# Performance work log

Measured on AMD Instinct MI355X. Metric: run time of the kernel, lower is better.

The kernel has to match this reference:

```python
import jax, jax.numpy as jnp
import numpy as np

N, K, D, H = 8192, 32, 128, 256

def setup_inputs() -> dict:
    key = jax.random.key(0)
    ks = jax.random.split(key, 12)
    x = jax.random.normal(ks[0], (N, D), dtype=jnp.float32)
    chosen = jax.random.randint(ks[1], (N, K), 0, N, dtype=jnp.int32)
    # column 0 = the node's own index (matches neighbors[0] == current in the torch code)
    nbrs = jnp.concatenate([jnp.arange(N, dtype=jnp.int32)[:, None], chosen], axis=1)
    t = jax.random.normal(ks[2], (N,), dtype=jnp.float32)
    e_hat = jax.random.normal(ks[3], (N,), dtype=jnp.float32)
    def lin(k, fan_in, fan_out):
        k1, k2 = jax.random.split(k)
        s = 1.0 / np.sqrt(fan_in)
        W = jax.random.uniform(k1, (fan_in, fan_out), minval=-s, maxval=s, dtype=jnp.float32)
        bb = jax.random.uniform(k2, (fan_out,), minval=-s, maxval=s, dtype=jnp.float32)
        return W, bb
    W1, b1 = lin(ks[4], 2 * D, H)
    W2, b2 = lin(ks[5], H, H)
    W3, b3 = lin(ks[6], H, 1)
    b = jnp.float32(1.0)
    return {"x": x, "nbrs": nbrs, "t": t, "e_hat": e_hat,
            "W1": W1, "b1": b1, "W2": W2, "b2": b2, "W3": W3, "b3": b3, "b": b}

def reference(x, nbrs, t, e_hat, W1, b1, W2, b2, W3, b3, b):
    n, d = x.shape
    cur = nbrs[:, 0]          # [n] node's own index
    chosen = nbrs[:, 1:]      # [n, K] neighbor indices
    k = chosen.shape[1]
    z_i = x[cur]              # [n, d]
    z_j = x[chosen]           # [n, K, d] ragged gather (regular degree)
    z_concat = jnp.concatenate(
        [jnp.broadcast_to(z_i[:, None, :], (n, k, d)), z_j], axis=-1)  # [n, K, 2d]
    h = jax.nn.relu(z_concat @ W1 + b1)
    h = jax.nn.relu(h @ W2 + b2)
    mlp_neigh = (h @ W3 + b3)[..., 0]                     # [n, K]
    scores = jax.nn.softmax(b * jnp.abs(mlp_neigh), axis=1)  # per-node softmax
    prop_res = t[chosen] - e_hat[chosen]                  # [n, K]
    w = mlp_neigh * scores                                # [n, K]
    Y_pred = jnp.sum(prop_res * w, axis=1)                # [n]
    pairwise = jnp.zeros((n, n), dtype=x.dtype).at[cur[:, None], chosen].set(w)
    pairwise = pairwise.at[cur, cur].set(0.0)             # zero self-weight last, as in torch
    return Y_pred, pairwise
```

## Files before the change

kernel.cpp:

```cpp
#include <hip/hip_runtime.h>

typedef short s8v __attribute__((ext_vector_type(8)));
typedef float f4v __attribute__((ext_vector_type(4)));

#define NN 8192
#define KN 32
#define DD 128
#define HH 256

static __device__ __forceinline__ unsigned short f2bf(float f) {
    union { float f; unsigned u; } v; v.f = f;
    unsigned r = v.u + 0x7fffu + ((v.u >> 16) & 1u);
    return (unsigned short)(r >> 16);
}
static __device__ __forceinline__ float bf2f(unsigned short h) {
    union { unsigned u; float f; } v; v.u = ((unsigned)h) << 16;
    return v.f;
}

__global__ __launch_bounds__(256) void prep_kernel(
    const float* __restrict__ W1, const float* __restrict__ W2,
    unsigned short* __restrict__ W1sh, unsigned short* __restrict__ W1sl,
    unsigned short* __restrict__ W2s)
{
    int tid = blockIdx.x * 256 + threadIdx.x;
    if (tid < 128 * 512) {
        int k = tid >> 9;
        int n = tid & 511;
        float w = (n < 256) ? W1[k * 256 + n] : W1[(128 + k) * 256 + (n - 256)];
        unsigned short hi = f2bf(w);
        float lo = w - bf2f(hi);
        int idx = ((k >> 5) * 512 + n) * 32 + (k & 31);
        W1sh[idx] = hi;
        W1sl[idx] = f2bf(lo);
    } else {
        int t2 = tid - 128 * 512;
        int k = t2 >> 8;
        int n = t2 & 255;
        W2s[((k >> 5) * 256 + n) * 32 + (k & 31)] = f2bf(W2[k * 256 + n]);
    }
}

__global__ __launch_bounds__(256) void pq_kernel(
    const float* __restrict__ x, const unsigned short* __restrict__ W1sh,
    const unsigned short* __restrict__ W1sl, const float* __restrict__ b1,
    float* __restrict__ P, unsigned short* __restrict__ Q)
{
    __shared__ unsigned short Ah[64 * 136];
    __shared__ unsigned short Al[64 * 136];
    int t  = threadIdx.x;
    int r0 = blockIdx.x * 64;
    int n0 = blockIdx.y * 256;

    {
        int m   = (t & 15) | ((t >> 6) << 4);
        int seg = (t >> 4) & 3;
        const float* xr = x + (r0 + m) * DD + seg * 32;
        #pragma unroll
        for (int it = 0; it < 4; ++it) {
            f4v v0 = *(const f4v*)(xr + it * 8);
            f4v v1 = *(const f4v*)(xr + it * 8 + 4);
            s8v hh, ll;
            #pragma unroll
            for (int e = 0; e < 8; ++e) {
                float v = (e < 4) ? v0[e] : v1[e - 4];
                unsigned short hi = f2bf(v);
                hh[e] = (short)hi;
                ll[e] = (short)f2bf(v - bf2f(hi));
            }
            int c = seg * 32 + it * 8;
            *(s8v*)(Ah + m * 136 + c) = hh;
            *(s8v*)(Al + m * 136 + c) = ll;
        }
    }
    __syncthreads();

    int lane = t & 63, wn = t >> 6, l15 = lane & 15, q = lane >> 4;
    f4v acc[4][4];
    #pragma unroll
    for (int mt = 0; mt < 4; ++mt)
        #pragma unroll
        for (int nt = 0; nt < 4; ++nt) acc[mt][nt] = (f4v){0.f, 0.f, 0.f, 0.f};

    #pragma unroll
    for (int kt = 0; kt < 4; ++kt) {
        s8v ah[4], al[4], bh[4], bl[4];
        #pragma unroll
        for (int mt = 0; mt < 4; ++mt) {
            int m = mt * 16 + l15;
            ah[mt] = *(const s8v*)(Ah + m * 136 + kt * 32 + q * 8);
            al[mt] = *(const s8v*)(Al + m * 136 + kt * 32 + q * 8);
        }
        #pragma unroll
        for (int nt = 0; nt < 4; ++nt) {
            int n = n0 + wn * 64 + nt * 16 + l15;
            int idx = (kt * 512 + n) * 32 + q * 8;
            bh[nt] = *(const s8v*)(W1sh + idx);
            bl[nt] = *(const s8v*)(W1sl + idx);
        }
        #pragma unroll
        for (int mt = 0; mt < 4; ++mt)
            #pragma unroll
            for (int nt = 0; nt < 4; ++nt) {
                acc[mt][nt] = __builtin_amdgcn_mfma_f32_16x16x32_bf16(ah[mt], bh[nt], acc[mt][nt], 0, 0, 0);
                acc[mt][nt] = __builtin_amdgcn_mfma_f32_16x16x32_bf16(ah[mt], bl[nt], acc[mt][nt], 0, 0, 0);
                acc[mt][nt] = __builtin_amdgcn_mfma_f32_16x16x32_bf16(al[mt], bh[nt], acc[mt][nt], 0, 0, 0);
            }
    }

    #pragma unroll
    for (int nt = 0; nt < 4; ++nt) {
        int cg = n0 + wn * 64 + nt * 16 + l15;
        if (cg < 256) {
            float bias = b1[cg];
            #pragma unroll
            for (int mt = 0; mt < 4; ++mt)
                #pragma unroll
                for (int r = 0; r < 4; ++r) {
                    int row = r0 + mt * 16 + q * 4 + r;
                    P[row * 256 + cg] = acc[mt][nt][r] + bias;
                }
        } else {
            int cq = cg - 256;
            #pragma unroll
            for (int mt = 0; mt < 4; ++mt)
                #pragma unroll
                for (int r = 0; r < 4; ++r) {
                    int row = r0 + mt * 16 + q * 4 + r;
                    Q[row * 256 + cq] = f2bf(acc[mt][nt][r]);
                }
        }
    }
}

__global__ __launch_bounds__(256) void main_kernel(
    const float* __restrict__ P, const unsigned short* __restrict__ Q,
    const unsigned short* __restrict__ W2s,
    const float* __restrict__ b2, const float* __restrict__ W3,
    const int* __restrict__ nbrs, const float* __restrict__ t_arr,
    const float* __restrict__ e_hat, const float* __restrict__ b3p,
    const float* __restrict__ bscal, float* __restrict__ out)
{
    __shared__ unsigned short A[64 * 264];
    __shared__ float mlpbuf[64][4];
    __shared__ float wbuf_w[2][32];
    __shared__ int   wbuf_j[2][32];
    int t = threadIdx.x;
    int node0 = blockIdx.x * 2;
    float* PW = out + NN;

    {
        int m   = (t & 15) | ((t >> 6) << 4);
        int seg = (t >> 4) & 3;
        int g = node0 + (m >> 5);
        int i = nbrs[g * 33];
        int j = nbrs[g * 33 + 1 + (m & 31)];
        const float* Pr = P + i * 256 + seg * 64;
        const unsigned short* Qr = Q + j * 256 + seg * 64;
        #pragma unroll
        for (int it = 0; it < 8; ++it) {
            f4v p0 = *(const f4v*)(Pr + it * 8);
            f4v p1 = *(const f4v*)(Pr + it * 8 + 4);
            s8v qv = *(const s8v*)(Qr + it * 8);
            s8v hv;
            #pragma unroll
            for (int e = 0; e < 8; ++e) {
                float pv = (e < 4) ? p0[e] : p1[e - 4];
                float v = pv + bf2f((unsigned short)qv[e]);
                v = v > 0.f ? v : 0.f;
                hv[e] = (short)f2bf(v);
            }
            *(s8v*)(A + m * 264 + seg * 64 + it * 8) = hv;
        }
    }
    __syncthreads();

    int lane = t & 63, wn = t >> 6, l15 = lane & 15, q = lane >> 4;
    f4v acc[4][4];
    #pragma unroll
    for (int mt = 0; mt < 4; ++mt)
        #pragma unroll
        for (int nt = 0; nt < 4; ++nt) acc[mt][nt] = (f4v){0.f, 0.f, 0.f, 0.f};

    #pragma unroll
    for (int kt = 0; kt < 8; ++kt) {
        s8v a[4], b[4];
        #pragma unroll
        for (int mt = 0; mt < 4; ++mt)
            a[mt] = *(const s8v*)(A + (mt * 16 + l15) * 264 + kt * 32 + q * 8);
        #pragma unroll
        for (int nt = 0; nt < 4; ++nt) {
            int n = wn * 64 + nt * 16 + l15;
            b[nt] = *(const s8v*)(W2s + (kt * 256 + n) * 32 + q * 8);
        }
        #pragma unroll
        for (int mt = 0; mt < 4; ++mt)
            #pragma unroll
            for (int nt = 0; nt < 4; ++nt)
                acc[mt][nt] = __builtin_amdgcn_mfma_f32_16x16x32_bf16(a[mt], b[nt], acc[mt][nt], 0, 0, 0);
    }

    float p[4][4];
    #pragma unroll
    for (int mt = 0; mt < 4; ++mt)
        #pragma unroll
        for (int r = 0; r < 4; ++r) p[mt][r] = 0.f;
    #pragma unroll
    for (int nt = 0; nt < 4; ++nt) {
        int c = wn * 64 + nt * 16 + l15;
        float bb = b2[c], w3 = W3[c];
        #pragma unroll
        for (int mt = 0; mt < 4; ++mt)
            #pragma unroll
            for (int r = 0; r < 4; ++r) {
                float v = acc[mt][nt][r] + bb;
                v = v > 0.f ? v : 0.f;
                p[mt][r] += v * w3;
            }
    }
    #pragma unroll
    for (int off = 1; off < 16; off <<= 1)
        #pragma unroll
        for (int mt = 0; mt < 4; ++mt)
            #pragma unroll
            for (int r = 0; r < 4; ++r)
                p[mt][r] += __shfl_xor(p[mt][r], off, 64);
    if (l15 == 0) {
        #pragma unroll
        for (int mt = 0; mt < 4; ++mt)
            #pragma unroll
            for (int r = 0; r < 4; ++r)
                mlpbuf[mt * 16 + q * 4 + r][wn] = p[mt][r];
    }
    __syncthreads();

    if (t < 128) {
        int node = t >> 6;
        int k = t & 63;
        if (k < 32) {
            int g = node0 + node;
            int m = node * 32 + k;
            float mlp = mlpbuf[m][0] + mlpbuf[m][1] + mlpbuf[m][2] + mlpbuf[m][3] + b3p[0];
            float aabs = bscal[0] * fabsf(mlp);
            float amax = aabs;
            #pragma unroll
            for (int off = 1; off < 32; off <<= 1)
                amax = fmaxf(amax, __shfl_xor(amax, off, 64));
            float e = __expf(aabs - amax);
            float s = e;
            #pragma unroll
            for (int off = 1; off < 32; off <<= 1)
                s += __shfl_xor(s, off, 64);
            float w = mlp * (e / s);

            int j = nbrs[g * 33 + 1 + k];
            float prop = t_arr[j] - e_hat[j];
            float yp = prop * w;
            #pragma unroll
            for (int off = 1; off < 32; off <<= 1)
                yp += __shfl_xor(yp, off, 64);
            if (k == 0) out[g] = yp;

            int curg = nbrs[g * 33];
            bool write = (j != curg);
            for (int kk = 0; kk < 32; ++kk) {
                int jv = __shfl(j, kk, 64);
                if (kk > k && jv == j) write = false;
            }
            wbuf_w[node][k] = w;
            wbuf_j[node][k] = write ? j : -1;
        }
    }
    __syncthreads();

    float* img = (float*)A;
    #pragma unroll 1
    for (int row = 0; row < 2; ++row) {
        f4v z = (f4v){0.f, 0.f, 0.f, 0.f};
        #pragma unroll
        for (int i = 0; i < 8; ++i)
            *(f4v*)(img + t * 4 + i * 1024) = z;
        __syncthreads();
        if (t < 32) {
            int j = wbuf_j[row][t];
            if (j >= 0) img[j] = wbuf_w[row][t];
        }
        __syncthreads();
        int cur = nbrs[(node0 + row) * 33];
        float* dst = PW + (long)cur * NN;
        #pragma unroll
        for (int i = 0; i < 8; ++i) {
            f4v v = *(const f4v*)(img + t * 4 + i * 1024);
            __builtin_nontemporal_store(v, (f4v*)(dst + t * 4 + i * 1024));
        }
    }
}

extern "C" void kernel_launch(void* const* d_in, const int* in_sizes, int n_in,
                              void* d_out, int out_size, void* d_ws, size_t ws_size,
                              hipStream_t stream) {
    const float* x     = (const float*)d_in[0];
    const int*   nbrs  = (const int*)d_in[1];
    const float* t     = (const float*)d_in[2];
    const float* e_hat = (const float*)d_in[3];
    const float* W1    = (const float*)d_in[4];
    const float* b1    = (const float*)d_in[5];
    const float* W2    = (const float*)d_in[6];
    const float* b2    = (const float*)d_in[7];
    const float* W3    = (const float*)d_in[8];
    const float* b3    = (const float*)d_in[9];
    const float* b     = (const float*)d_in[10];

    char* ws = (char*)d_ws;
    float*          P     = (float*)ws;
    unsigned short* Q     = (unsigned short*)(ws + 8388608);
    unsigned short* W1sh  = (unsigned short*)(ws + 12582912);
    unsigned short* W1sl  = (unsigned short*)(ws + 12713984);
    unsigned short* W2s   = (unsigned short*)(ws + 12845056);

    prep_kernel<<<512, 256, 0, stream>>>(W1, W2, W1sh, W1sl, W2s);
    pq_kernel<<<dim3(128, 2), 256, 0, stream>>>(x, W1sh, W1sl, b1, P, Q);
    main_kernel<<<4096, 256, 0, stream>>>(P, Q, W2s, b2, W3, nbrs, t, e_hat,
                                          b3, b, (float*)d_out);
}
```

Before: 353.0 us.

## Split dense pairwise-matrix write into a separate streaming kernel

The main kernel now stores per-node neighbor indices and weights to a workspace instead of materializing and streaming the 8192-wide pairwise rows itself. A new write_kernel, one block per node, zero-fills a 32KB shared image, scatters the weights, and streams the row out with nontemporal stores. This separates the compute-bound MLP phase from the bandwidth-bound 256MB output write so each kernel can run at its own occupancy. The cost is an extra launch and a small workspace round trip, and write_kernel's 32KB of shared memory may cap how many blocks fit per CU.

```diff
diff --git a/kernel.cpp b/kernel.cpp
--- a/kernel.cpp
+++ b/kernel.cpp
@@ -139,15 +139,13 @@
     const float* __restrict__ b2, const float* __restrict__ W3,
     const int* __restrict__ nbrs, const float* __restrict__ t_arr,
     const float* __restrict__ e_hat, const float* __restrict__ b3p,
-    const float* __restrict__ bscal, float* __restrict__ out)
+    const float* __restrict__ bscal, int* __restrict__ wj,
+    float* __restrict__ ww, float* __restrict__ out)
 {
     __shared__ unsigned short A[64 * 264];
     __shared__ float mlpbuf[64][4];
-    __shared__ float wbuf_w[2][32];
-    __shared__ int   wbuf_j[2][32];
     int t = threadIdx.x;
     int node0 = blockIdx.x * 2;
-    float* PW = out + NN;
 
     {
         int m   = (t & 15) | ((t >> 6) << 4);
@@ -267,32 +265,37 @@
                 int jv = __shfl(j, kk, 64);
                 if (kk > k && jv == j) write = false;
             }
-            wbuf_w[node][k] = w;
-            wbuf_j[node][k] = write ? j : -1;
-        }
-    }
-    __syncthreads();
-
-    float* img = (float*)A;
-    #pragma unroll 1
-    for (int row = 0; row < 2; ++row) {
-        f4v z = (f4v){0.f, 0.f, 0.f, 0.f};
-        #pragma unroll
-        for (int i = 0; i < 8; ++i)
-            *(f4v*)(img + t * 4 + i * 1024) = z;
-        __syncthreads();
-        if (t < 32) {
-            int j = wbuf_j[row][t];
-            if (j >= 0) img[j] = wbuf_w[row][t];
-        }
-        __syncthreads();
-        int cur = nbrs[(node0 + row) * 33];
-        float* dst = PW + (long)cur * NN;
-        #pragma unroll
-        for (int i = 0; i < 8; ++i) {
-            f4v v = *(const f4v*)(img + t * 4 + i * 1024);
-            __builtin_nontemporal_store(v, (f4v*)(dst + t * 4 + i * 1024));
-        }
+            wj[g * 32 + k] = write ? j : -1;
+            ww[g * 32 + k] = w;
+        }
+    }
+}
+
+__global__ __launch_bounds__(256) void write_kernel(
+    const int* __restrict__ wj, const float* __restrict__ ww,
+    const int* __restrict__ nbrs, float* __restrict__ out)
+{
+    __shared__ float img[NN];
+    int t = threadIdx.x;
+    int g = blockIdx.x;
+
+    int j = -1; float w = 0.f;
+    if (t < 32) { j = wj[g * 32 + t]; w = ww[g * 32 + t]; }
+
+    f4v z = (f4v){0.f, 0.f, 0.f, 0.f};
+    #pragma unroll
+    for (int i = 0; i < 8; ++i)
+        *(f4v*)(img + t * 4 + i * 1024) = z;
+    __syncthreads();
+    if (j >= 0) img[j] = w;
+    __syncthreads();
+
+    int cur = nbrs[g * 33];
+    float* dst = out + NN + (long)cur * NN;
+    #pragma unroll
+    for (int i = 0; i < 8; ++i) {
+        f4v v = *(const f4v*)(img + t * 4 + i * 1024);
+        __builtin_nontemporal_store(v, (f4v*)(dst + t * 4 + i * 1024));
     }
 }
 
@@ -317,9 +320,12 @@
     unsigned short* W1sh  = (unsigned short*)(ws + 12582912);
     unsigned short* W1sl  = (unsigned short*)(ws + 12713984);
     unsigned short* W2s   = (unsigned short*)(ws + 12845056);
+    int*            wj    = (int*)(ws + 12976128);
+    float*          ww    = (float*)(ws + 14024704);
 
     prep_kernel<<<512, 256, 0, stream>>>(W1, W2, W1sh, W1sl, W2s);
     pq_kernel<<<dim3(128, 2), 256, 0, stream>>>(x, W1sh, W1sl, b1, P, Q);
     main_kernel<<<4096, 256, 0, stream>>>(P, Q, W2s, b2, W3, nbrs, t, e_hat,
-                                          b3, b, (float*)d_out);
-}
+                                          b3, b, wj, ww, (float*)d_out);
+    write_kernel<<<8192, 256, 0, stream>>>(wj, ww, nbrs, (float*)d_out);
+}
```

Result: slower. 373.3 us (+5.8%).
